# Optimization experiments

Hardware: AMD Instinct MI355X
Metric: run time of the kernel (lower is better)

## Reference

```python
import jax, jax.numpy as jnp
import numpy as np


def _gru_cell(x, h, Wih, Whh, bih, bhh):
    # PyTorch GRU cell (seq_len=1): gates ordered r, z, n
    gi = x @ Wih.T + bih
    gh = h @ Whh.T + bhh
    i_r, i_z, i_n = jnp.split(gi, 3, axis=-1)
    h_r, h_z, h_n = jnp.split(gh, 3, axis=-1)
    r = jax.nn.sigmoid(i_r + h_r)
    z = jax.nn.sigmoid(i_z + h_z)
    n = jnp.tanh(i_n + r * h_n)
    return (1.0 - z) * n + z * h


def setup_inputs() -> dict:
    key = jax.random.key(0)
    N, K, n_in, H = 4096, 8, 14, 128
    ks = jax.random.split(key, 24)
    s = 0.05
    inp = {
        "towers": jax.random.normal(ks[0], (N, K, n_in), jnp.float32),
        # E_n encoder (Linear -> tanh -> Linear -> tanh)
        "En_W1": jax.random.normal(ks[1], (H, n_in)) * s,
        "En_b1": jnp.zeros((H,)),
        "En_W2": jax.random.normal(ks[2], (H, H)) * s,
        "En_b2": jnp.zeros((H,)),
        # E_e encoder
        "Ee_W1": jax.random.normal(ks[3], (H, 2 * n_in)) * s,
        "Ee_b1": jnp.zeros((H,)),
        "Ee_W2": jax.random.normal(ks[4], (H, H)) * s,
        "Ee_b2": jnp.zeros((H,)),
        # U_gru (node update), input n_in + H
        "U_Wih": jax.random.normal(ks[5], (3 * H, n_in + H)) * s,
        "U_Whh": jax.random.normal(ks[6], (3 * H, H)) * s,
        "U_bih": jnp.zeros((3 * H,)),
        "U_bhh": jnp.zeros((3 * H,)),
        # M_gru (edge update), input 2*(n_in + H)
        "M_Wih": jax.random.normal(ks[7], (3 * H, 2 * (n_in + H))) * s,
        "M_Whh": jax.random.normal(ks[8], (3 * H, H)) * s,
        "M_bih": jnp.zeros((3 * H,)),
        "M_bhh": jnp.zeros((3 * H,)),
        # G_gru (global update), input 2*H
        "G_Wih": jax.random.normal(ks[9], (3 * H, 2 * H)) * s,
        "G_Whh": jax.random.normal(ks[10], (3 * H, H)) * s,
        "G_bih": jnp.zeros((3 * H,)),
        "G_bhh": jnp.zeros((3 * H,)),
        # output head
        "O_W": jax.random.normal(ks[11], (1, H)) * s,
        "O_b": jnp.zeros((1,)),
        "k": 3,
    }
    return inp


def reference(towers, En_W1, En_b1, En_W2, En_b2, Ee_W1, Ee_b1, Ee_W2, Ee_b2,
              U_Wih, U_Whh, U_bih, U_bhh, M_Wih, M_Whh, M_bih, M_bhh,
              G_Wih, G_Whh, G_bih, G_bhh, O_W, O_b, k):
    N, K, n_in = towers.shape
    H = En_W1.shape[0]
    # node state init: h = E_n(towers)
    h = jnp.tanh(jnp.tanh(towers @ En_W1.T + En_b1) @ En_W2.T + En_b2)  # (N,K,H)
    # edge state init: e_h = E_e(all-pairs concat of towers)
    xi = jnp.broadcast_to(towers[:, :, None, :], (N, K, K, n_in))
    xj = jnp.broadcast_to(towers[:, None, :, :], (N, K, K, n_in))
    xx0 = jnp.concatenate([xi, xj], axis=-1)  # (N,K,K,2*n_in)
    e_h = jnp.tanh(jnp.tanh(xx0 @ Ee_W1.T + Ee_b1) @ Ee_W2.T + Ee_b2)  # (N,K,K,H)
    # mask[i,j] = 1 iff j == i+1 (the nested-loop mask is a shifted identity)
    mask = jnp.eye(K, k=1, dtype=towers.dtype)
    e = e_h
    D = n_in + H
    for _ in range(k):
        # edge_fn: all-pairs concat of [towers, h] fed through GRU cell
        xh = jnp.concatenate([towers, h], axis=-1)  # (N,K,D)
        a = jnp.broadcast_to(xh[:, :, None, :], (N, K, K, D))
        b = jnp.broadcast_to(xh[:, None, :, :], (N, K, K, D))
        exx = jnp.concatenate([a, b], axis=-1).reshape(-1, 2 * D)
        e_h = _gru_cell(exx, e_h.reshape(-1, H), M_Wih, M_Whh, M_bih, M_bhh)
        e = e_h.reshape(N, K, K, H)
        # node_fn: masked sum selects e[:, i, i+1]
        edges = jnp.einsum('nijh,ij->nih', e, mask)  # (N,K,H)
        nx = jnp.concatenate([towers, edges], axis=-1).reshape(-1, D)
        h = _gru_cell(nx, h.reshape(-1, H), U_Wih, U_Whh, U_bih, U_bhh).reshape(N, K, H)
        e_h = e_h  # state carried
    # global_fn
    h_sum = h.sum(axis=1)  # (N,H)
    e_sum = jnp.einsum('nijh,ij->nh', e, mask)  # (N,H)
    gx = jnp.concatenate([h_sum, e_sum], axis=-1)  # (N,2H)
    g = _gru_cell(gx, jnp.zeros((N, H), towers.dtype), G_Wih, G_Whh, G_bih, G_bhh)
    out = jax.nn.sigmoid((g @ O_W.T + O_b).reshape(N))
    return out
```

## Files before the change

### kernel.cpp

```cpp
#include <hip/hip_runtime.h>
#include <hip/hip_bf16.h>

typedef __hip_bfloat16 bf16;
typedef unsigned short ush;
typedef short s16x8 __attribute__((ext_vector_type(8)));
typedef ush u16x4 __attribute__((ext_vector_type(4)));
typedef float f32x4 __attribute__((ext_vector_type(4)));

#define DEV __device__ __forceinline__

DEV float rcp_f(float x) { return __builtin_amdgcn_rcpf(x); }
DEV float sigmoid_f(float x) { return rcp_f(1.f + __expf(-x)); }
DEV float tanh_f(float x) { return 1.f - 2.f * rcp_f(__expf(2.f * x) + 1.f); }

DEV float u2f(ush u) { unsigned int v = ((unsigned int)u) << 16; float f; __builtin_memcpy(&f, &v, 4); return f; }
DEV ush f2u(float f) { bf16 h = __float2bfloat16(f); ush u; __builtin_memcpy(&u, &h, 2); return u; }

DEV f32x4 MFMA(s16x8 a, s16x8 b, f32x4 c) {
  return __builtin_amdgcn_mfma_f32_16x16x32_bf16(a, b, c, 0, 0, 0);
}

DEV s16x8 z8() {
  s16x8 v;
  for (int z = 0; z < 8; ++z) v[z] = 0;
  return v;
}

DEV int swz_idx(int row, int kk) { return row * 32 + (((kk >> 3) ^ ((row >> 1) & 3)) << 3) + (kk & 7); }
DEV int swz_blk(int row, int blk) { return row * 32 + ((blk ^ ((row >> 1) & 3)) << 3); }


__global__ __launch_bounds__(256) void prep_all(
    const float* __restrict__ towers,
    const float* __restrict__ MWih, const float* __restrict__ MWhh,
    const float* __restrict__ UWih, const float* __restrict__ UWhh,
    const float* __restrict__ EnW1, const float* __restrict__ EnW2,
    const float* __restrict__ EeW1, const float* __restrict__ EeW2,
    const float* __restrict__ MBih, const float* __restrict__ MBhh,
    const float* __restrict__ UBih, const float* __restrict__ UBhh,
    const float* __restrict__ GWih, const float* __restrict__ GWhh,
    const float* __restrict__ GBih, const float* __restrict__ GBhh,
    ush* __restrict__ xh, ush* __restrict__ WIHe, ush* __restrict__ WTh,
    ush* __restrict__ WTu, ush* __restrict__ WBen1, ush* __restrict__ WBen2,
    ush* __restrict__ WBee1, ush* __restrict__ WBee2,
    float* __restrict__ biasM, float* __restrict__ biasU,
    float* __restrict__ WT_G, float* __restrict__ biasG)
{
  const int b = blockIdx.x, t = threadIdx.x;
  if (b < 2048) {
    const int idx = b * 256 + t;
    const int row = idx >> 4, kk = idx & 15;
    xh[row * 144 + kk] = f2u(kk < 14 ? towers[row * 14 + kk] : 0.f);
  } else if (b < 2480) {
    const int idx = (b - 2048) * 256 + t;
    const int ck = idx / 12288, rem = idx % 12288, n = rem >> 5, kk = rem & 31;
    const int k = ck * 32 + kk;
    const int gate = n >> 7, c = n & 127;
    const int row = gate * 128 + c;
    int col = -1;
    if (k < 14)                    col = k;
    else if (k >= 16 && k < 144)   col = 14 + (k - 16);
    else if (k >= 144 && k < 158)  col = 142 + (k - 144);
    else if (k >= 160)             col = 156 + (k - 160);
    WIHe[idx] = f2u((col >= 0) ? MWih[row * 284 + col] : 0.f);
  } else if (b < 2672) {
    const int idx = (b - 2480) * 256 + t;
    const int ck = idx / 12288, rem = idx % 12288, n = rem >> 5, kk = rem & 31;
    const int g = n >> 7, c = n & 127;
    WTh[idx] = f2u(MWhh[(g * 128 + c) * 128 + ck * 32 + kk]);
  } else if (b < 3248) {
    const int idx = (b - 2672) * 256 + t;
    const int ck = idx >> 14, n = (idx >> 5) & 511, kk = idx & 31;
    const int k = ck * 32 + kk, gate = n >> 7, c = n & 127;
    float w = 0.f;
    const int row = (gate == 0) ? c : (gate == 1) ? 128 + c : 256 + c;
    if (k < 160) {
      int col = -1;
      if (k < 16)        { if (k < 14) col = k; }
      else if (k < 144)  col = 14 + (k - 16);
      if (gate != 3 && col >= 0) w = UWih[row * 142 + col];
    } else {
      if (gate != 2) w = UWhh[row * 128 + (k - 160)];
    }
    WTu[ck * 16384 + swz_idx(n, kk)] = f2u(w);
  } else if (b < 3264) {
    const int idx = (b - 3248) * 256 + t;
    const int n = (idx >> 5) & 127, kk = idx & 31;
    WBen1[idx] = f2u(kk < 14 ? EnW1[n * 14 + kk] : 0.f);
  } else if (b < 3328) {
    const int idx = (b - 3264) * 256 + t;
    const int ck = idx >> 12, n = (idx >> 5) & 127, kk = idx & 31;
    WBen2[idx] = f2u(EnW2[n * 128 + ck * 32 + kk]);
  } else if (b < 3344) {
    const int idx = (b - 3328) * 256 + t;
    const int n = (idx >> 5) & 127, kk = idx & 31;
    int col = (kk < 16) ? (kk < 14 ? kk : -1) : (kk < 30 ? 14 + (kk - 16) : -1);
    WBee1[idx] = f2u(col >= 0 ? EeW1[n * 28 + col] : 0.f);
    (void)n;
  } else if (b < 3408) {
    const int idx = (b - 3344) * 256 + t;
    const int ck = idx >> 12, n = (idx >> 5) & 127, kk = idx & 31;
    WBee2[idx] = f2u(EeW2[n * 128 + ck * 32 + kk]);
  } else if (b < 3410) {
    const int idx = (b - 3408) * 256 + t;
    const int g = idx >> 7, c = idx & 127;
    float v;
    if (g == 0)      v = MBih[c] + MBhh[c];
    else if (g == 1) v = MBih[128 + c] + MBhh[128 + c];
    else if (g == 2) v = MBih[256 + c];
    else             v = MBhh[256 + c];
    biasM[idx] = v;
  } else if (b < 3412) {
    const int idx = (b - 3410) * 256 + t;
    const int g = idx >> 7, c = idx & 127;
    float v;
    if (g == 0)      v = UBih[c] + UBhh[c];
    else if (g == 1) v = UBih[128 + c] + UBhh[128 + c];
    else if (g == 2) v = UBih[256 + c];
    else             v = UBhh[256 + c];
    biasU[idx] = v;
  } else if (b < 4180) {
    const int idx = (b - 3412) * 256 + t;
    const int kc = idx >> 9, cg = (idx >> 2) & 127, gate = idx & 3;
    const int row = (gate == 0) ? cg : (gate == 1) ? cg + 128 : cg + 256;
    float v = 0.f;
    if (kc < 256) { if (gate != 3) v = GWih[row * 256 + kc]; }
    else          { if (gate != 2) v = GWhh[row * 128 + (kc - 256)]; }
    WT_G[idx] = v;
  } else {
    const int idx = (b - 4180) * 256 + t;
    const int cg = idx >> 2, gate = idx & 3;
    float v;
    if (gate == 0)      v = GBih[cg] + GBhh[cg];
    else if (gate == 1) v = GBih[cg + 128] + GBhh[cg + 128];
    else if (gate == 2) v = GBih[cg + 256];
    else                v = GBhh[cg + 256];
    biasG[idx] = v;
  }
}

__global__ __launch_bounds__(256, 2) void enc_en(
    ush* __restrict__ xh,
    const ush* __restrict__ WB1, const float* __restrict__ b1,
    const ush* __restrict__ WB2, const float* __restrict__ b2)
{
  __shared__ ush smem[9216];
  ush* A1 = smem;
  ush* Z1 = smem + 1024;
  const int t = threadIdx.x, lane = t & 63, w = t >> 6;
  const int rowBase = blockIdx.x * 64;
  const int quad = lane >> 4, l15 = lane & 15;

  {
    const int gm = t >> 2, gb = t & 3, grow = rowBase + gm;
    s16x8 v = z8();
    if (gb < 2) v = *(const s16x8*)(xh + grow * 144 + gb * 8);
    *(s16x8*)&A1[swz_blk(gm, gb)] = v;
  }
  __syncthreads();

  s16x8 af[4];
  #pragma unroll
  for (int rt = 0; rt < 4; ++rt)
    af[rt] = *(const s16x8*)&A1[swz_blk(rt * 16 + l15, quad)];
  f32x4 acc1[4][2];
  #pragma unroll
  for (int rt = 0; rt < 4; ++rt)
    #pragma unroll
    for (int ct = 0; ct < 2; ++ct) {
      #pragma unroll
      for (int q = 0; q < 4; ++q) acc1[rt][ct][q] = 0.f;
    }
  #pragma unroll
  for (int ct = 0; ct < 2; ++ct) {
    const int n = w * 32 + ct * 16 + l15;
    const s16x8 bf = *(const s16x8*)&WB1[n * 32 + quad * 8];
    #pragma unroll
    for (int rt = 0; rt < 4; ++rt) acc1[rt][ct] = MFMA(af[rt], bf, acc1[rt][ct]);
  }
  #pragma unroll
  for (int ct = 0; ct < 2; ++ct) {
    const int col = w * 32 + ct * 16 + l15;
    const int kk = col & 31;
    #pragma unroll
    for (int rt = 0; rt < 4; ++rt) {
      #pragma unroll
      for (int q = 0; q < 4; ++q) {
        const int m = rt * 16 + quad * 4 + q;
        Z1[w * 2048 + swz_idx(m, kk)] = f2u(tanh_f(acc1[rt][ct][q] + b1[col]));
      }
    }
  }
  __syncthreads();

  f32x4 acc2[4][2];
  #pragma unroll
  for (int rt = 0; rt < 4; ++rt)
    #pragma unroll
    for (int ct = 0; ct < 2; ++ct) {
      #pragma unroll
      for (int q = 0; q < 4; ++q) acc2[rt][ct][q] = 0.f;
    }
  for (int ck2 = 0; ck2 < 4; ++ck2) {
    #pragma unroll
    for (int rt = 0; rt < 4; ++rt)
      af[rt] = *(const s16x8*)&Z1[ck2 * 2048 + swz_blk(rt * 16 + l15, quad)];
    #pragma unroll
    for (int ct = 0; ct < 2; ++ct) {
      const int n = w * 32 + ct * 16 + l15;
      const s16x8 bf = *(const s16x8*)&WB2[(ck2 * 128 + n) * 32 + quad * 8];
      #pragma unroll
      for (int rt = 0; rt < 4; ++rt) acc2[rt][ct] = MFMA(af[rt], bf, acc2[rt][ct]);
    }
  }

  #pragma unroll
  for (int ct = 0; ct < 2; ++ct) {
    const int col = w * 32 + ct * 16 + l15;
    #pragma unroll
    for (int rt = 0; rt < 4; ++rt) {
      #pragma unroll
      for (int q = 0; q < 4; ++q) {
        const int r = rt * 16 + quad * 4 + q;
        xh[(rowBase + r) * 144 + 16 + col] = f2u(tanh_f(acc2[rt][ct][q] + b2[col]));
      }
    }
  }
}

DEV void ee_body(ush* As_e, ush* SC, const ush* __restrict__ xh,
                 const ush* __restrict__ WB1, const float* __restrict__ b1,
                 const ush* __restrict__ WB2, const float* __restrict__ b2,
                 int G0, int t)
{
  ush* A1 = SC;
  ush* Z1 = SC + 1024;
  const int lane = t & 63, w = t >> 6;
  const int quad = lane >> 4, l15 = lane & 15;

  {
    const int gm = t >> 2, gb = t & 3;
    const int gg = gm >> 3, i = gm & 7;
    const int xi = (G0 + gg) * 8 + i;
    const int xj = (i < 7) ? xi + 1 : xi;
    const s16x8 v = (gb < 2) ? *(const s16x8*)(xh + xi * 144 + gb * 8)
                             : *(const s16x8*)(xh + xj * 144 + (gb - 2) * 8);
    *(s16x8*)&A1[swz_blk(gm, gb)] = v;
  }
  __syncthreads();

  s16x8 af[4];
  #pragma unroll
  for (int rt = 0; rt < 4; ++rt)
    af[rt] = *(const s16x8*)&A1[swz_blk(rt * 16 + l15, quad)];
  f32x4 acc1[4][2];
  #pragma unroll
  for (int rt = 0; rt < 4; ++rt)
    #pragma unroll
    for (int ct = 0; ct < 2; ++ct) {
      #pragma unroll
      for (int q = 0; q < 4; ++q) acc1[rt][ct][q] = 0.f;
    }
  #pragma unroll
  for (int ct = 0; ct < 2; ++ct) {
    const int n = w * 32 + ct * 16 + l15;
    const s16x8 bf = *(const s16x8*)&WB1[n * 32 + quad * 8];
    #pragma unroll
    for (int rt = 0; rt < 4; ++rt) acc1[rt][ct] = MFMA(af[rt], bf, acc1[rt][ct]);
  }
  #pragma unroll
  for (int ct = 0; ct < 2; ++ct) {
    const int col = w * 32 + ct * 16 + l15;
    const int kk = col & 31;
    #pragma unroll
    for (int rt = 0; rt < 4; ++rt) {
      #pragma unroll
      for (int q = 0; q < 4; ++q) {
        const int m = rt * 16 + quad * 4 + q;
        Z1[w * 2048 + swz_idx(m, kk)] = f2u(tanh_f(acc1[rt][ct][q] + b1[col]));
      }
    }
  }
  __syncthreads();

  f32x4 acc2[4][2];
  #pragma unroll
  for (int rt = 0; rt < 4; ++rt)
    #pragma unroll
    for (int ct = 0; ct < 2; ++ct) {
      #pragma unroll
      for (int q = 0; q < 4; ++q) acc2[rt][ct][q] = 0.f;
    }
  for (int ck2 = 0; ck2 < 4; ++ck2) {
    #pragma unroll
    for (int rt = 0; rt < 4; ++rt)
      af[rt] = *(const s16x8*)&Z1[ck2 * 2048 + swz_blk(rt * 16 + l15, quad)];
    #pragma unroll
    for (int ct = 0; ct < 2; ++ct) {
      const int n = w * 32 + ct * 16 + l15;
      const s16x8 bf = *(const s16x8*)&WB2[(ck2 * 128 + n) * 32 + quad * 8];
      #pragma unroll
      for (int rt = 0; rt < 4; ++rt) acc2[rt][ct] = MFMA(af[rt], bf, acc2[rt][ct]);
    }
  }
  #pragma unroll
  for (int ct = 0; ct < 2; ++ct) {
    const int col = w * 32 + ct * 16 + l15;
    const int kk = col & 31;
    #pragma unroll
    for (int rt = 0; rt < 4; ++rt) {
      #pragma unroll
      for (int q = 0; q < 4; ++q) {
        const int r = rt * 16 + quad * 4 + q;
        As_e[(col >> 5) * 2048 + swz_idx(r, kk)] = f2u(tanh_f(acc2[rt][ct][q] + b2[col]));
      }
    }
  }
}

DEV void edge_gru_core(const ush* As_e, ush* Bxx, ush* __restrict__ eh,
                       const ush* __restrict__ WIHe, const ush* __restrict__ WTh,
                       const float* __restrict__ biasM,
                       const ush* __restrict__ xh, int G0, int t)
{
  const int lane = t & 63, w = t >> 6;
  const int quad = lane >> 4, l15 = lane & 15;
  const int ko = quad * 8;

  f32x4 accR[2][4], accZ[2][4], accN1[2][4], accN2[2][4];
  #pragma unroll
  for (int mt = 0; mt < 2; ++mt)
    #pragma unroll
    for (int nt = 0; nt < 4; ++nt) {
      #pragma unroll
      for (int q = 0; q < 4; ++q) { accR[mt][nt][q] = 0.f; accZ[mt][nt][q] = 0.f; accN1[mt][nt][q] = 0.f; accN2[mt][nt][q] = 0.f; }
    }

  auto stage_xx = [&](int ck) {
    const int gm = t >> 2, gb = t & 3;
    const int gg = gm >> 3, i = gm & 7;
    const int xi = (G0 + gg) * 8 + i;
    const int xj = xi + ((i < 7) ? 1 : 0);
    const int k0 = ck * 32 + gb * 8;
    const s16x8 v = (k0 < 144) ? *(const s16x8*)(xh + xi * 144 + k0)
                               : *(const s16x8*)(xh + xj * 144 + (k0 - 144));
    *(s16x8*)&Bxx[(ck & 1) * 2048 + swz_blk(gm, gb)] = v;
  };

  stage_xx(0);
  __syncthreads();
  for (int ck = 0; ck < 9; ++ck) {
    if (ck + 1 < 9) stage_xx(ck + 1);
    const ush* Bc = Bxx + (ck & 1) * 2048;
    s16x8 be[4];
    #pragma unroll
    for (int nt = 0; nt < 4; ++nt)
      be[nt] = *(const s16x8*)&Bc[swz_blk(nt * 16 + l15, quad)];
    #pragma unroll
    for (int mt = 0; mt < 2; ++mt) {
      const int nb = w * 32 + mt * 16 + l15;
      const s16x8 aR = *(const s16x8*)&WIHe[(ck * 384 + nb) * 32 + ko];
      const s16x8 aZ = *(const s16x8*)&WIHe[(ck * 384 + 128 + nb) * 32 + ko];
      const s16x8 aN = *(const s16x8*)&WIHe[(ck * 384 + 256 + nb) * 32 + ko];
      #pragma unroll
      for (int nt = 0; nt < 4; ++nt) {
        accR[mt][nt]  = MFMA(aR, be[nt], accR[mt][nt]);
        accZ[mt][nt]  = MFMA(aZ, be[nt], accZ[mt][nt]);
        accN1[mt][nt] = MFMA(aN, be[nt], accN1[mt][nt]);
      }
    }
    __syncthreads();
  }

  #pragma unroll
  for (int ck = 0; ck < 4; ++ck) {
    s16x8 be[4];
    #pragma unroll
    for (int nt = 0; nt < 4; ++nt)
      be[nt] = *(const s16x8*)&As_e[ck * 2048 + swz_blk(nt * 16 + l15, quad)];
    #pragma unroll
    for (int mt = 0; mt < 2; ++mt) {
      const int nb = w * 32 + mt * 16 + l15;
      const s16x8 aR = *(const s16x8*)&WTh[(ck * 384 + nb) * 32 + ko];
      const s16x8 aZ = *(const s16x8*)&WTh[(ck * 384 + 128 + nb) * 32 + ko];
      const s16x8 aN = *(const s16x8*)&WTh[(ck * 384 + 256 + nb) * 32 + ko];
      #pragma unroll
      for (int nt = 0; nt < 4; ++nt) {
        accR[mt][nt]  = MFMA(aR, be[nt], accR[mt][nt]);
        accZ[mt][nt]  = MFMA(aZ, be[nt], accZ[mt][nt]);
        accN2[mt][nt] = MFMA(aN, be[nt], accN2[mt][nt]);
      }
    }
  }

  #pragma unroll
  for (int mt = 0; mt < 2; ++mt) {
    const int hc0 = w * 32 + mt * 16 + quad * 4;
    const int ck2 = hc0 >> 5, kkB = hc0 & 31;
    #pragma unroll
    for (int nt = 0; nt < 4; ++nt) {
      const int erow = nt * 16 + l15;
      const int gg = erow >> 3, i = erow & 7;
      if (i == 7) continue;
      const u16x4 hp4 = *(const u16x4*)&As_e[ck2 * 2048 + swz_blk(erow, kkB >> 3) + (kkB & 7)];
      u16x4 ov;
      #pragma unroll
      for (int q = 0; q < 4; ++q) {
        const int c = hc0 + q;
        const float rg = sigmoid_f(accR[mt][nt][q] + biasM[c]);
        const float zg = sigmoid_f(accZ[mt][nt][q] + biasM[128 + c]);
        const float nn = tanh_f(accN1[mt][nt][q] + biasM[256 + c]
                                + rg * (accN2[mt][nt][q] + biasM[384 + c]));
        const float hp = u2f(hp4[q]);
        ov[q] = f2u(nn + zg * (hp - nn));
      }
      *(u16x4*)&eh[(size_t)((G0 + gg) * 64 + i * 9 + 1) * 128 + hc0] = ov;
    }
  }
}

__global__ __launch_bounds__(256, 2) void edge_first(
    ush* __restrict__ eh, const ush* __restrict__ WIHe,
    const ush* __restrict__ WTh, const float* __restrict__ biasM,
    const ush* __restrict__ xh,
    const ush* __restrict__ WB1, const float* __restrict__ b1,
    const ush* __restrict__ WB2, const float* __restrict__ b2)
{
  __shared__ ush smem[17408];
  ush* As_e = smem;
  ush* SC   = smem + 8192;
  const int t = threadIdx.x;
  const int G0 = blockIdx.x * 8;

  ee_body(As_e, SC, xh, WB1, b1, WB2, b2, G0, t);
  __syncthreads();
  edge_gru_core(As_e, SC, eh, WIHe, WTh, biasM, xh, G0, t);
}

__global__ __launch_bounds__(256, 2) void edge_next(
    ush* __restrict__ eh, const ush* __restrict__ WIHe,
    const ush* __restrict__ WTh, const float* __restrict__ biasM,
    const ush* __restrict__ xh)
{
  __shared__ ush smem[12288];
  ush* As_e = smem;
  ush* Bxx  = smem + 8192;
  const int t = threadIdx.x;
  const int G0 = blockIdx.x * 8;

  {
    const int gm = t >> 2, gb = t & 3;
    const int gg = gm >> 3, i = gm & 7;
    const ush* src = eh + (size_t)((G0 + gg) * 64 + i * 9 + 1) * 128;
    #pragma unroll
    for (int ck = 0; ck < 4; ++ck) {
      s16x8 v = z8();
      if (i < 7) v = *(const s16x8*)(src + ck * 32 + gb * 8);
      *(s16x8*)&As_e[ck * 2048 + swz_blk(gm, gb)] = v;
    }
  }
  __syncthreads();

  edge_gru_core(As_e, Bxx, eh, WIHe, WTh, biasM, xh, G0, t);
}

__global__ __launch_bounds__(256, 2) void gru_node(
    ush* __restrict__ xh, const ush* __restrict__ eh,
    const ush* __restrict__ WT, const float* __restrict__ bias)
{
  constexpr int NCH = 9, XCH = 5;
  __shared__ ush smem[4096];
  const int t = threadIdx.x, lane = t & 63, w = t >> 6;
  const int rowBase = blockIdx.x * 64;
  const int gm = t >> 2, gb = t & 3, grow = rowBase + gm;
  const int l15 = lane & 15, quad = lane >> 4;

  f32x4 accR[4][2], accZ[4][2], accN1[4][2], accN2[4][2];
  #pragma unroll
  for (int rt = 0; rt < 4; ++rt)
    #pragma unroll
    for (int s = 0; s < 2; ++s) {
      #pragma unroll
      for (int q = 0; q < 4; ++q) { accR[rt][s][q] = 0.f; accZ[rt][s][q] = 0.f; accN1[rt][s][q] = 0.f; accN2[rt][s][q] = 0.f; }
    }

  auto stage = [&](int ck) {
    const int k0 = ck * 32 + gb * 8;
    s16x8 v = z8();
    if (k0 < 16)       v = *(const s16x8*)(xh + grow * 144 + k0);
    else if (k0 < 144) {
      const int i = grow & 7;
      if (i < 7) v = *(const s16x8*)(eh + (size_t)(grow * 8 + i + 1) * 128 + (k0 - 16));
    } else if (k0 >= 160) {
      v = *(const s16x8*)(xh + grow * 144 + 16 + (k0 - 160));
    }
    *(s16x8*)&smem[(ck & 1) * 2048 + swz_blk(gm, gb)] = v;
  };

  stage(0);
  __syncthreads();

  for (int ck = 0; ck < NCH; ++ck) {
    if (ck + 1 < NCH) stage(ck + 1);

    const ush* Wc = WT + ck * 16384;
    const ush* Ac = smem + (ck & 1) * 2048;
    s16x8 af[4];
    #pragma unroll
    for (int rt = 0; rt < 4; ++rt)
      af[rt] = *(const s16x8*)&Ac[swz_blk(rt * 16 + l15, quad)];
    if (ck < XCH) {
      #pragma unroll
      for (int s = 0; s < 2; ++s) {
        const int nb = w * 32 + s * 16 + l15;
        const s16x8 bR = *(const s16x8*)&Wc[swz_blk(0 * 128 + nb, quad)];
        const s16x8 bZ = *(const s16x8*)&Wc[swz_blk(1 * 128 + nb, quad)];
        const s16x8 bN = *(const s16x8*)&Wc[swz_blk(2 * 128 + nb, quad)];
        #pragma unroll
        for (int rt = 0; rt < 4; ++rt) {
          accR[rt][s]  = MFMA(af[rt], bR, accR[rt][s]);
          accZ[rt][s]  = MFMA(af[rt], bZ, accZ[rt][s]);
          accN1[rt][s] = MFMA(af[rt], bN, accN1[rt][s]);
        }
      }
    } else {
      #pragma unroll
      for (int s = 0; s < 2; ++s) {
        const int nb = w * 32 + s * 16 + l15;
        const s16x8 bR = *(const s16x8*)&Wc[swz_blk(0 * 128 + nb, quad)];
        const s16x8 bZ = *(const s16x8*)&Wc[swz_blk(1 * 128 + nb, quad)];
        const s16x8 bN = *(const s16x8*)&Wc[swz_blk(3 * 128 + nb, quad)];
        #pragma unroll
        for (int rt = 0; rt < 4; ++rt) {
          accR[rt][s]  = MFMA(af[rt], bR, accR[rt][s]);
          accZ[rt][s]  = MFMA(af[rt], bZ, accZ[rt][s]);
          accN2[rt][s] = MFMA(af[rt], bN, accN2[rt][s]);
        }
      }
    }
    __syncthreads();
  }

  #pragma unroll
  for (int s = 0; s < 2; ++s) {
    const int hcol = w * 32 + s * 16 + l15;
    const float bR = bias[hcol], bZ = bias[128 + hcol], bN1 = bias[256 + hcol], bN2 = bias[384 + hcol];
    #pragma unroll
    for (int rt = 0; rt < 4; ++rt) {
      #pragma unroll
      for (int q = 0; q < 4; ++q) {
        const int r = rt * 16 + quad * 4 + q;
        const int row = rowBase + r;
        const float hp = u2f(xh[row * 144 + 16 + hcol]);
        const float rg = sigmoid_f(accR[rt][s][q] + bR);
        const float zg = sigmoid_f(accZ[rt][s][q] + bZ);
        const float nn = tanh_f(accN1[rt][s][q] + bN1 + rg * (accN2[rt][s][q] + bN2));
        xh[row * 144 + 16 + hcol] = f2u(nn + zg * (hp - nn));
      }
    }
  }
}

__global__ __launch_bounds__(256) void sums2(const ush* __restrict__ xh, const ush* __restrict__ eh,
                                             float* __restrict__ hsum, float* __restrict__ esum) {
  const int idx = blockIdx.x * 256 + threadIdx.x;
  const int n = idx >> 7, hh = idx & 127;
  float hs = 0.f, es = 0.f;
  #pragma unroll
  for (int i = 0; i < 8; ++i) hs += u2f(xh[(n * 8 + i) * 144 + 16 + hh]);
  #pragma unroll
  for (int i = 0; i < 7; ++i) es += u2f(eh[(size_t)((n * 8 + i) * 8 + i + 1) * 128 + hh]);
  hsum[idx] = hs;
  esum[idx] = es;
}

__global__ __launch_bounds__(256) void gru_global_out(
    const float* __restrict__ hsum, const float* __restrict__ esum,
    const float* __restrict__ WT, const float* __restrict__ bias,
    const float* __restrict__ OW, const float* __restrict__ Ob,
    float* __restrict__ out)
{
  constexpr int KT = 384;
  __shared__ float4 ATl4[KT * 4];
  __shared__ float4 Bl4[16 * 128];
  __shared__ float gmat[16 * 128];
  __shared__ float red[16 * 4];
  float* ATl = (float*)ATl4;
  const int t = threadIdx.x;
  const int rowBase = blockIdx.x * 16;
  for (int idx = t; idx < KT * 16; idx += 256) {
    const int kc = idx >> 4, r = idx & 15, grow = rowBase + r;
    float v = 0.f;
    if (kc < 128)      v = hsum[grow * 128 + kc];
    else if (kc < 256) v = esum[grow * 128 + (kc - 128)];
    ATl[idx] = v;
  }
  const int c = t & 127, rh = t >> 7;
  float accR[8], accZ[8], accN1[8];
  #pragma unroll
  for (int rr = 0; rr < 8; ++rr) { accR[rr] = 0.f; accZ[rr] = 0.f; accN1[rr] = 0.f; }
  const float4* WT4 = (const float4*)WT;
  for (int ck = 0; ck < 16; ++ck) {
    __syncthreads();
    #pragma unroll
    for (int ii = 0; ii < 8; ++ii) { const int idx = t + ii * 256; Bl4[idx] = WT4[ck * 2048 + idx]; }
    __syncthreads();
    const int kb = ck * 16;
    #pragma unroll
    for (int kcl = 0; kcl < 16; ++kcl) {
      const float4 wv = Bl4[kcl * 128 + c];
      const float4 a0 = ATl4[(kb + kcl) * 4 + rh * 2];
      const float4 a1 = ATl4[(kb + kcl) * 4 + rh * 2 + 1];
      const float av[8] = {a0.x, a0.y, a0.z, a0.w, a1.x, a1.y, a1.z, a1.w};
      #pragma unroll
      for (int rr = 0; rr < 8; ++rr) {
        accR[rr]  += wv.x * av[rr];
        accZ[rr]  += wv.y * av[rr];
        accN1[rr] += wv.z * av[rr];
      }
    }
  }
  const float4 bb = ((const float4*)bias)[c];
  const float ow = OW[c];
  #pragma unroll
  for (int rr = 0; rr < 8; ++rr) {
    const float rg = sigmoid_f(accR[rr] + bb.x);
    const float zg = sigmoid_f(accZ[rr] + bb.y);
    const float nn = tanh_f(accN1[rr] + bb.z + rg * bb.w);
    gmat[(rh * 8 + rr) * 128 + c] = (1.f - zg) * nn * ow;
  }
  __syncthreads();
  if (t < 64) {
    const int r = t >> 2, part = t & 3;
    float s = 0.f;
    #pragma unroll
    for (int cc = 0; cc < 32; ++cc) s += gmat[r * 128 + part * 32 + cc];
    red[r * 4 + part] = s;
  }
  __syncthreads();
  if (t < 16) {
    const float s = red[t * 4] + red[t * 4 + 1] + red[t * 4 + 2] + red[t * 4 + 3];
    out[rowBase + t] = sigmoid_f(s + Ob[0]);
  }
}

extern "C" void kernel_launch(void* const* d_in, const int* in_sizes, int n_in,
                              void* d_out, int out_size, void* d_ws, size_t ws_size,
                              hipStream_t stream)
{
  (void)in_sizes; (void)n_in; (void)out_size; (void)ws_size;
  const float* towers = (const float*)d_in[0];
  const float* EnW1 = (const float*)d_in[1];
  const float* EnB1 = (const float*)d_in[2];
  const float* EnW2 = (const float*)d_in[3];
  const float* EnB2 = (const float*)d_in[4];
  const float* EeW1 = (const float*)d_in[5];
  const float* EeB1 = (const float*)d_in[6];
  const float* EeW2 = (const float*)d_in[7];
  const float* EeB2 = (const float*)d_in[8];
  const float* UWih = (const float*)d_in[9];
  const float* UWhh = (const float*)d_in[10];
  const float* UBih = (const float*)d_in[11];
  const float* UBhh = (const float*)d_in[12];
  const float* MWih = (const float*)d_in[13];
  const float* MWhh = (const float*)d_in[14];
  const float* MBih = (const float*)d_in[15];
  const float* MBhh = (const float*)d_in[16];
  const float* GWih = (const float*)d_in[17];
  const float* GWhh = (const float*)d_in[18];
  const float* GBih = (const float*)d_in[19];
  const float* GBhh = (const float*)d_in[20];
  const float* OW   = (const float*)d_in[21];
  const float* Ob   = (const float*)d_in[22];

  char* ws = (char*)d_ws;
  size_t off = 0;
  auto take = [&](size_t b) { void* p = ws + off; off = (off + b + 255) & ~(size_t)255; return p; };
  ush*   xh     = (ush*)take((size_t)32768 * 144 * 2);
  ush*   eh     = (ush*)take((size_t)262144 * 128 * 2);
  float* hsum   = (float*)take((size_t)4096 * 128 * 4);
  float* esum   = (float*)take((size_t)4096 * 128 * 4);
  ush*   WIHe   = (ush*)take((size_t)9 * 384 * 32 * 2);
  ush*   WTh    = (ush*)take((size_t)4 * 384 * 32 * 2);
  ush*   WTu    = (ush*)take((size_t)9 * 512 * 32 * 2);
  ush*   WBen1  = (ush*)take((size_t)128 * 32 * 2);
  ush*   WBen2  = (ush*)take((size_t)4 * 128 * 32 * 2);
  ush*   WBee1  = (ush*)take((size_t)128 * 32 * 2);
  ush*   WBee2  = (ush*)take((size_t)4 * 128 * 32 * 2);
  float* biasM  = (float*)take(512 * 4);
  float* biasU  = (float*)take(512 * 4);
  float* WT_G   = (float*)take((size_t)384 * 512 * 4);
  float* biasG  = (float*)take(512 * 4);

  prep_all<<<4182, 256, 0, stream>>>(
      towers, MWih, MWhh, UWih, UWhh, EnW1, EnW2, EeW1, EeW2,
      MBih, MBhh, UBih, UBhh, GWih, GWhh, GBih, GBhh,
      xh, WIHe, WTh, WTu, WBen1, WBen2, WBee1, WBee2,
      biasM, biasU, WT_G, biasG);

  enc_en<<<512, 256, 0, stream>>>(xh, WBen1, EnB1, WBen2, EnB2);

  edge_first<<<512, 256, 0, stream>>>(eh, WIHe, WTh, biasM, xh, WBee1, EeB1, WBee2, EeB2);
  gru_node<<<512, 256, 0, stream>>>(xh, eh, WTu, biasU);
  edge_next<<<512, 256, 0, stream>>>(eh, WIHe, WTh, biasM, xh);
  gru_node<<<512, 256, 0, stream>>>(xh, eh, WTu, biasU);
  edge_next<<<512, 256, 0, stream>>>(eh, WIHe, WTh, biasM, xh);
  gru_node<<<512, 256, 0, stream>>>(xh, eh, WTu, biasU);

  sums2<<<2048, 256, 0, stream>>>(xh, eh, hsum, esum);
  gru_global_out<<<256, 256, 0, stream>>>(hsum, esum, WT_G, biasG, OW, Ob, (float*)d_out);
}
```

Before: 257.8 us.

## Fuse edge GRU, node GRU and sums into one kernel per iteration

Merges the edge-update kernel, node-update kernel and the final sums kernel into one templated kernel per message-passing iteration. The new edge state stays in shared memory and is consumed there by the node GRU and the sums, so eh round-trips through global memory are avoided, and on the last iteration eh is not written at all. This cuts kernel launches from seven to three and removes global reads of the diagonal edges. In exchange it adds block-level syncs and keeps more shared memory live per block, which may affect occupancy.

Result: faster. 244.5 us (-5.2%).

```diff
diff --git a/kernel.cpp b/kernel.cpp
--- a/kernel.cpp
+++ b/kernel.cpp
@@ -318,10 +318,11 @@
   }
 }
 
-DEV void edge_gru_core(const ush* As_e, ush* Bxx, ush* __restrict__ eh,
-                       const ush* __restrict__ WIHe, const ush* __restrict__ WTh,
-                       const float* __restrict__ biasM,
-                       const ush* __restrict__ xh, int G0, int t)
+template<int LAST>
+DEV void edge_core(ush* As_e, ush* Bxx, ush* __restrict__ eh,
+                   const ush* __restrict__ WIHe, const ush* __restrict__ WTh,
+                   const float* __restrict__ biasM,
+                   const ush* __restrict__ xh, int G0, int t)
 {
   const int lane = t & 63, w = t >> 6;
   const int quad = lane >> 4, l15 = lane & 15;
@@ -393,6 +394,8 @@
     }
   }
 
+  __syncthreads();
+
   #pragma unroll
   for (int mt = 0; mt < 2; ++mt) {
     const int hc0 = w * 32 + mt * 16 + quad * 4;
@@ -401,8 +404,8 @@
     for (int nt = 0; nt < 4; ++nt) {
       const int erow = nt * 16 + l15;
       const int gg = erow >> 3, i = erow & 7;
-      if (i == 7) continue;
-      const u16x4 hp4 = *(const u16x4*)&As_e[ck2 * 2048 + swz_blk(erow, kkB >> 3) + (kkB & 7)];
+      ush* cell = &As_e[ck2 * 2048 + swz_blk(erow, kkB >> 3) + (kkB & 7)];
+      const u16x4 hp4 = *(const u16x4*)cell;
       u16x4 ov;
       #pragma unroll
       for (int q = 0; q < 4; ++q) {
@@ -414,64 +417,19 @@
         const float hp = u2f(hp4[q]);
         ov[q] = f2u(nn + zg * (hp - nn));
       }
-      *(u16x4*)&eh[(size_t)((G0 + gg) * 64 + i * 9 + 1) * 128 + hc0] = ov;
-    }
-  }
-}
-
-__global__ __launch_bounds__(256, 2) void edge_first(
-    ush* __restrict__ eh, const ush* __restrict__ WIHe,
-    const ush* __restrict__ WTh, const float* __restrict__ biasM,
-    const ush* __restrict__ xh,
-    const ush* __restrict__ WB1, const float* __restrict__ b1,
-    const ush* __restrict__ WB2, const float* __restrict__ b2)
-{
-  __shared__ ush smem[17408];
-  ush* As_e = smem;
-  ush* SC   = smem + 8192;
-  const int t = threadIdx.x;
-  const int G0 = blockIdx.x * 8;
-
-  ee_body(As_e, SC, xh, WB1, b1, WB2, b2, G0, t);
-  __syncthreads();
-  edge_gru_core(As_e, SC, eh, WIHe, WTh, biasM, xh, G0, t);
-}
-
-__global__ __launch_bounds__(256, 2) void edge_next(
-    ush* __restrict__ eh, const ush* __restrict__ WIHe,
-    const ush* __restrict__ WTh, const float* __restrict__ biasM,
-    const ush* __restrict__ xh)
-{
-  __shared__ ush smem[12288];
-  ush* As_e = smem;
-  ush* Bxx  = smem + 8192;
-  const int t = threadIdx.x;
-  const int G0 = blockIdx.x * 8;
-
-  {
-    const int gm = t >> 2, gb = t & 3;
-    const int gg = gm >> 3, i = gm & 7;
-    const ush* src = eh + (size_t)((G0 + gg) * 64 + i * 9 + 1) * 128;
-    #pragma unroll
-    for (int ck = 0; ck < 4; ++ck) {
-      s16x8 v = z8();
-      if (i < 7) v = *(const s16x8*)(src + ck * 32 + gb * 8);
-      *(s16x8*)&As_e[ck * 2048 + swz_blk(gm, gb)] = v;
-    }
-  }
-  __syncthreads();
-
-  edge_gru_core(As_e, Bxx, eh, WIHe, WTh, biasM, xh, G0, t);
-}
-
-__global__ __launch_bounds__(256, 2) void gru_node(
-    ush* __restrict__ xh, const ush* __restrict__ eh,
-    const ush* __restrict__ WT, const float* __restrict__ bias)
+      *(u16x4*)cell = ov;
+      if (!LAST && i < 7)
+        *(u16x4*)&eh[(size_t)((G0 + gg) * 64 + i * 9 + 1) * 128 + hc0] = ov;
+    }
+  }
+}
+
+DEV void node_lds(const ush* As_e, ush* SC, ush* __restrict__ xh,
+                  const ush* __restrict__ WT, const float* __restrict__ bias,
+                  int rowBase, int t)
 {
   constexpr int NCH = 9, XCH = 5;
-  __shared__ ush smem[4096];
-  const int t = threadIdx.x, lane = t & 63, w = t >> 6;
-  const int rowBase = blockIdx.x * 64;
+  const int lane = t & 63, w = t >> 6;
   const int gm = t >> 2, gb = t & 3, grow = rowBase + gm;
   const int l15 = lane & 15, quad = lane >> 4;
 
@@ -489,12 +447,15 @@
     s16x8 v = z8();
     if (k0 < 16)       v = *(const s16x8*)(xh + grow * 144 + k0);
     else if (k0 < 144) {
-      const int i = grow & 7;
-      if (i < 7) v = *(const s16x8*)(eh + (size_t)(grow * 8 + i + 1) * 128 + (k0 - 16));
+      const int i = gm & 7;
+      if (i < 7) {
+        const int ke = k0 - 16;
+        v = *(const s16x8*)&As_e[(ke >> 5) * 2048 + swz_blk(gm, (ke & 31) >> 3)];
+      }
     } else if (k0 >= 160) {
       v = *(const s16x8*)(xh + grow * 144 + 16 + (k0 - 160));
     }
-    *(s16x8*)&smem[(ck & 1) * 2048 + swz_blk(gm, gb)] = v;
+    *(s16x8*)&SC[(ck & 1) * 2048 + swz_blk(gm, gb)] = v;
   };
 
   stage(0);
@@ -504,7 +465,7 @@
     if (ck + 1 < NCH) stage(ck + 1);
 
     const ush* Wc = WT + ck * 16384;
-    const ush* Ac = smem + (ck & 1) * 2048;
+    const ush* Ac = SC + (ck & 1) * 2048;
     s16x8 af[4];
     #pragma unroll
     for (int rt = 0; rt < 4; ++rt)
@@ -561,17 +522,69 @@
   }
 }
 
-__global__ __launch_bounds__(256) void sums2(const ush* __restrict__ xh, const ush* __restrict__ eh,
-                                             float* __restrict__ hsum, float* __restrict__ esum) {
-  const int idx = blockIdx.x * 256 + threadIdx.x;
-  const int n = idx >> 7, hh = idx & 127;
-  float hs = 0.f, es = 0.f;
-  #pragma unroll
-  for (int i = 0; i < 8; ++i) hs += u2f(xh[(n * 8 + i) * 144 + 16 + hh]);
-  #pragma unroll
-  for (int i = 0; i < 7; ++i) es += u2f(eh[(size_t)((n * 8 + i) * 8 + i + 1) * 128 + hh]);
-  hsum[idx] = hs;
-  esum[idx] = es;
+DEV void sums_body(const ush* As_e, const ush* __restrict__ xh,
+                   float* __restrict__ hsum, float* __restrict__ esum,
+                   int G0, int rowBase, int t)
+{
+  #pragma unroll
+  for (int ii = 0; ii < 4; ++ii) {
+    const int p = t + ii * 256;
+    const int gg = p >> 7, hh = p & 127;
+    float es = 0.f;
+    #pragma unroll
+    for (int i = 0; i < 7; ++i) {
+      const int slot = gg * 8 + i;
+      es += u2f(As_e[(hh >> 5) * 2048 + swz_idx(slot, hh & 31)]);
+    }
+    float hs = 0.f;
+    #pragma unroll
+    for (int i = 0; i < 8; ++i)
+      hs += u2f(xh[(rowBase + gg * 8 + i) * 144 + 16 + hh]);
+    hsum[(G0 + gg) * 128 + hh] = hs;
+    esum[(G0 + gg) * 128 + hh] = es;
+  }
+}
+
+template<int FIRST, int LAST>
+__global__ __launch_bounds__(256, 2) void gn_iter(
+    ush* __restrict__ eh, ush* __restrict__ xh,
+    const ush* __restrict__ WIHe, const ush* __restrict__ WTh,
+    const float* __restrict__ biasM,
+    const ush* __restrict__ WTu, const float* __restrict__ biasU,
+    const ush* __restrict__ WBee1, const float* __restrict__ bEe1,
+    const ush* __restrict__ WBee2, const float* __restrict__ bEe2,
+    float* __restrict__ hsum, float* __restrict__ esum)
+{
+  __shared__ ush smem[17408];
+  ush* As_e = smem;
+  ush* SC   = smem + 8192;
+  const int t = threadIdx.x;
+  const int G0 = blockIdx.x * 8, rowBase = blockIdx.x * 64;
+
+  if (FIRST) {
+    ee_body(As_e, SC, xh, WBee1, bEe1, WBee2, bEe2, G0, t);
+  } else {
+    const int gm = t >> 2, gb = t & 3;
+    const int gg = gm >> 3, i = gm & 7;
+    const ush* src = eh + (size_t)((G0 + gg) * 64 + i * 9 + 1) * 128;
+    #pragma unroll
+    for (int ck = 0; ck < 4; ++ck) {
+      s16x8 v = z8();
+      if (i < 7) v = *(const s16x8*)(src + ck * 32 + gb * 8);
+      *(s16x8*)&As_e[ck * 2048 + swz_blk(gm, gb)] = v;
+    }
+  }
+  __syncthreads();
+
+  edge_core<LAST>(As_e, SC, eh, WIHe, WTh, biasM, xh, G0, t);
+  __syncthreads();
+
+  node_lds(As_e, SC, xh, WTu, biasU, rowBase, t);
+
+  if (LAST) {
+    __syncthreads();
+    sums_body(As_e, xh, hsum, esum, G0, rowBase, t);
+  }
 }
 
 __global__ __launch_bounds__(256) void gru_global_out(
@@ -700,13 +713,12 @@
 
   enc_en<<<512, 256, 0, stream>>>(xh, WBen1, EnB1, WBen2, EnB2);
 
-  edge_first<<<512, 256, 0, stream>>>(eh, WIHe, WTh, biasM, xh, WBee1, EeB1, WBee2, EeB2);
-  gru_node<<<512, 256, 0, stream>>>(xh, eh, WTu, biasU);
-  edge_next<<<512, 256, 0, stream>>>(eh, WIHe, WTh, biasM, xh);
-  gru_node<<<512, 256, 0, stream>>>(xh, eh, WTu, biasU);
-  edge_next<<<512, 256, 0, stream>>>(eh, WIHe, WTh, biasM, xh);
-  gru_node<<<512, 256, 0, stream>>>(xh, eh, WTu, biasU);
-
-  sums2<<<2048, 256, 0, stream>>>(xh, eh, hsum, esum);
+  gn_iter<1, 0><<<512, 256, 0, stream>>>(eh, xh, WIHe, WTh, biasM, WTu, biasU,
+                                         WBee1, EeB1, WBee2, EeB2, hsum, esum);
+  gn_iter<0, 0><<<512, 256, 0, stream>>>(eh, xh, WIHe, WTh, biasM, WTu, biasU,
+                                         WBee1, EeB1, WBee2, EeB2, hsum, esum);
+  gn_iter<0, 1><<<512, 256, 0, stream>>>(eh, xh, WIHe, WTh, biasM, WTu, biasU,
+                                         WBee1, EeB1, WBee2, EeB2, hsum, esum);
+
   gru_global_out<<<256, 256, 0, stream>>>(hsum, esum, WT_G, biasG, OW, Ob, (float*)d_out);
 }
```
